# Kernel tuning notes

Measured on AMD Instinct MI355X. Metric: run time of the kernel, lower is better.

The kernel has to match this reference:

```python
import jax, jax.numpy as jnp
import numpy as np

N, F, DEG, C = 20000, 64, 16, 16   # nodes, features, in-degree incl. self loop, classes
E = N * (DEG - 1)                   # regular (non-self-loop) edges


def setup_inputs() -> dict:
    key = jax.random.key(0)
    ks = jax.random.split(key, 12)
    x = jax.random.normal(ks[0], (N, F), dtype=jnp.float32)
    src = jax.random.randint(ks[1], (E,), 0, N, dtype=jnp.int32)
    dst = jnp.repeat(jnp.arange(N, dtype=jnp.int32), DEG - 1)  # exactly DEG-1 in-edges/node
    edge_index = jnp.stack([src, dst])
    s = 1.0 / np.sqrt(F)
    params = {}
    for i, kw, kb in ((1, ks[2], ks[3]), (2, ks[4], ks[5]), (3, ks[6], ks[7])):
        params[f"W{i}"] = jax.random.normal(kw, (F, F), dtype=jnp.float32) * s
        params[f"b{i}"] = jax.random.normal(kb, (F,), dtype=jnp.float32) * s
    params["Wfc"] = jax.random.normal(ks[8], (C, F), dtype=jnp.float32) * s
    params["bfc"] = jax.random.normal(ks[9], (C,), dtype=jnp.float32) * s
    return {"x": x, "edge_index": edge_index, **params}


def _pca_conv(h, src, dst, W, b):
    # GCNConv.forward: linear first, then propagate with symmetric normalization.
    hl = h @ W.T                                             # [N, F]
    # add self loops (appended after regular edges, as in PyG)
    loop = jnp.arange(N, dtype=src.dtype)
    src_a = jnp.concatenate([src, loop])
    dst_a = jnp.concatenate([dst, loop])
    deg = jnp.zeros((N,), hl.dtype).at[dst_a].add(1.0)
    dinv = jax.lax.rsqrt(deg)
    norm = dinv[src_a] * dinv[dst_a]                         # [Ea]
    m = norm[:, None] * hl[src_a]                            # messages [Ea, F]
    # aggregate(): pack each destination's messages contiguously, in edge order
    order = jnp.argsort(dst_a)                               # stable sort by destination
    sd = dst_a[order]
    slot = jnp.arange(sd.shape[0]) - jnp.searchsorted(sd, sd, side='left')
    neigh = jnp.zeros((N, DEG, F), hl.dtype).at[sd, slot].set(m[order])
    neigh = neigh.reshape(N, DEG * F)                        # [N, max_degree*F]
    # torch.pca_lowrank(neigh, q=F, center=True): top-F right singular vectors of
    # the column-centered matrix; computed via eigh on the (DEG*F x DEG*F) Gram.
    Xc = neigh - jnp.mean(neigh, axis=0, keepdims=True)
    G = Xc.T @ Xc                                            # [DEG*F, DEG*F]
    _, V = jnp.linalg.eigh(G)                                # ascending eigenvalues
    Vtop = V[:, ::-1][:, :F]                                 # top-F principal directions
    proj = neigh @ Vtop                                      # note: projects UNcentered neigh
    return proj @ W.T + b                                    # self.lin again + bias


def reference(x, edge_index, W1, b1, W2, b2, W3, b3, Wfc, bfc):
    src, dst = edge_index[0], edge_index[1]
    h = jax.nn.relu(_pca_conv(x, src, dst, W1, b1))
    h = jax.nn.relu(_pca_conv(h, src, dst, W2, b2))
    h = jax.nn.relu(_pca_conv(h, src, dst, W3, b3))
    out = h @ Wfc.T + bfc
    return jax.nn.log_softmax(out, axis=-1)
```

## Files before the change

kernel.cpp:

```cpp
#include <hip/hip_runtime.h>
#include <cmath>

#define NNODES 20000
#define FD 64
#define EPN 15
#define NB 1024
#define BSUB 80
#define NCLS 16
#define NPAIR 40

__global__ __launch_bounds__(256) void k_linT(const float* __restrict__ X,
    const float* __restrict__ W, const float* __restrict__ bias,
    float* __restrict__ out, int ncol, int relu)
{
  __shared__ float Wsh[64][65];
  __shared__ float Xsh[64][65];
  int t = threadIdx.x;
  int r0 = blockIdx.x * 64;
  for (int idx = t; idx < ncol * 64; idx += 256) Wsh[idx >> 6][idx & 63] = W[idx];
  for (int idx = t; idx < 64 * 64; idx += 256) {
    int r = idx >> 6, c = idx & 63;
    Xsh[r][c] = (r0 + r < NNODES) ? X[(size_t)(r0 + r) * 64 + c] : 0.f;
  }
  __syncthreads();
  for (int idx = t; idx < 64 * ncol; idx += 256) {
    int r = idx / ncol, o = idx % ncol;
    float acc = 0.f;
    #pragma unroll
    for (int j = 0; j < 64; j++) acc += Xsh[r][j] * Wsh[o][j];
    if (bias) acc += bias[o];
    if (relu) acc = fmaxf(acc, 0.f);
    if (r0 + r < NNODES) out[(size_t)(r0 + r) * ncol + o] = acc;
  }
}

__global__ __launch_bounds__(256) void k_meanslot(const float* __restrict__ hl,
    const int* __restrict__ src, float* __restrict__ mus)
{
  int k = blockIdx.x;
  int part = blockIdx.y;
  int t = threadIdx.x;
  int c = t & 63, sub = t >> 6;
  int d0 = part * 2500;
  float acc = 0.f;
  for (int d = d0 + sub; d < d0 + 2500; d += 4) {
    int row = (k < EPN) ? src[d * EPN + k] : d;
    acc += hl[(size_t)row * 64 + c];
  }
  __shared__ float red[4][64];
  red[sub][c] = acc;
  __syncthreads();
  if (t < 64) {
    float s = red[0][t] + red[1][t] + red[2][t] + red[3][t];
    atomicAdd(&mus[k * 64 + t], s * (1.f / 20000.f));
  }
}

__global__ __launch_bounds__(256) void k_buildX(const float* __restrict__ hl,
    const int* __restrict__ src, const float* __restrict__ mus,
    float* __restrict__ X)
{
  __shared__ float4 mu4[256];
  int t = threadIdx.x;
  int d0 = blockIdx.x * 64;
  mu4[t] = ((const float4*)mus)[t];
  __syncthreads();
  for (int k = 0; k < 16; k++) {
    for (int item = t; item < 1024; item += 256) {
      int rr = item >> 4, f4 = item & 15;
      int d = d0 + rr;
      if (d < NNODES) {
        int row = (k < EPN) ? src[d * EPN + k] : d;
        float4 v = ((const float4*)hl)[(size_t)row * 16 + f4];
        float4 m = mu4[k * 16 + f4];
        v.x -= m.x; v.y -= m.y; v.z -= m.z; v.w -= m.w;
        ((float4*)X)[(size_t)d * 256 + k * 16 + f4] = v;
      }
    }
  }
}

__global__ __launch_bounds__(256) void k_syrkX(const float* __restrict__ X,
    float* __restrict__ TP, int rows)
{
  __shared__ float As[32][128];
  __shared__ float Bs[32][128];
  int t = threadIdx.x;
  int pr = blockIdx.x, I = 0, rem = pr;
  for (int ii = 0; ii < 8; ii++) {
    int cnt = 8 - ii;
    if (rem < cnt) { I = ii; break; }
    rem -= cnt;
  }
  int J = I + rem;
  int d0 = blockIdx.y * rows;
  int d1 = d0 + rows;
  int a0 = (t & 15) * 4, b0 = (t >> 4) * 4;
  float4 pa[4], pb[4];
  auto LOADR = [&](int dc) {
    #pragma unroll
    for (int s = 0; s < 4; s++) {
      int idx = t + s * 256;
      int rr = idx >> 5, c4 = idx & 31;
      int d = dc + rr;
      float4 va = make_float4(0.f, 0.f, 0.f, 0.f), vb = va;
      if (d < d1) {
        va = ((const float4*)X)[(size_t)d * 256 + I * 32 + c4];
        vb = ((const float4*)X)[(size_t)d * 256 + J * 32 + c4];
      }
      pa[s] = va; pb[s] = vb;
    }
  };
  LOADR(d0);
  float acc[8][8] = {};
  for (int dc = d0; dc < d1; dc += 32) {
    __syncthreads();
    #pragma unroll
    for (int s = 0; s < 4; s++) {
      int idx = t + s * 256;
      int rr = idx >> 5, c4 = idx & 31;
      *(float4*)&As[rr][c4 * 4] = pa[s];
      *(float4*)&Bs[rr][c4 * 4] = pb[s];
    }
    __syncthreads();
    if (dc + 32 < d1) LOADR(dc + 32);
    for (int dd = 0; dd < 32; dd++) {
      float av[8], bv[8];
      *(float4*)&av[0] = *(const float4*)&As[dd][a0];
      *(float4*)&av[4] = *(const float4*)&As[dd][a0 + 64];
      *(float4*)&bv[0] = *(const float4*)&Bs[dd][b0];
      *(float4*)&bv[4] = *(const float4*)&Bs[dd][b0 + 64];
      #pragma unroll
      for (int x = 0; x < 8; x++)
        #pragma unroll
        for (int y = 0; y < 8; y++) acc[x][y] += av[x] * bv[y];
    }
  }
  float* Tout = TP + (size_t)blockIdx.y * ((size_t)NB * NB);
  #pragma unroll
  for (int x = 0; x < 8; x++) {
    int rowi = I * 128 + ((x < 4) ? (a0 + x) : (64 + a0 + x - 4));
    size_t base = (size_t)rowi * NB + J * 128;
    *(float4*)&Tout[base + b0]      = make_float4(acc[x][0], acc[x][1], acc[x][2], acc[x][3]);
    *(float4*)&Tout[base + 64 + b0] = make_float4(acc[x][4], acc[x][5], acc[x][6], acc[x][7]);
  }
}

__global__ __launch_bounds__(256) void k_assembleG16(const float* __restrict__ TP,
    float* __restrict__ G, int ns)
{
  size_t idx = (size_t)blockIdx.x * 256 + threadIdx.x;
  int p = (int)(idx >> 10), q = (int)(idx & 1023);
  int ti = p >> 6, tj = q >> 6;
  size_t e = (ti <= tj) ? idx : (((size_t)q << 10) | (size_t)p);
  float v = 0.f;
  for (int s2 = 0; s2 < ns; s2++) v += TP[(size_t)s2 * ((size_t)NB * NB) + e];
  G[idx] = v * (1.f / 256.f);
}

__global__ __launch_bounds__(256) void k_gram(const float* __restrict__ hl,
    const int* __restrict__ src, const float* __restrict__ mus,
    float* __restrict__ T)
{
  __shared__ float Ash[64][64];
  __shared__ float Bsh[64][64];
  __shared__ float muA[64], muB[64];
  int t = threadIdx.x;
  int pr = blockIdx.x, i = 0, rem = pr;
  for (int ii = 0; ii < 16; ii++) {
    int cnt = 16 - ii;
    if (rem < cnt) { i = ii; break; }
    rem -= cnt;
  }
  int j = i + rem;
  if (t < 64) muA[t] = mus[i * 64 + t];
  else if (t < 128) muB[t - 64] = mus[j * 64 + (t - 64)];
  float acc[4][4] = {};
  int a0 = (t & 15) * 4, b0 = (t >> 4) * 4;
  int d0 = blockIdx.y * 4000, d1 = d0 + 4000;
  for (int dc = d0; dc < d1; dc += 64) {
    __syncthreads();
    for (int item = t; item < 1024; item += 256) {
      int rr = item >> 4, f4 = item & 15;
      int d = dc + rr;
      float4 va = make_float4(0.f, 0.f, 0.f, 0.f);
      float4 vb = va;
      if (d < d1) {
        int ra = (i < EPN) ? src[d * EPN + i] : d;
        int rb = (j < EPN) ? src[d * EPN + j] : d;
        va = ((const float4*)hl)[(size_t)ra * 16 + f4];
        vb = ((const float4*)hl)[(size_t)rb * 16 + f4];
        int cb = f4 * 4;
        va.x -= muA[cb]; va.y -= muA[cb + 1]; va.z -= muA[cb + 2]; va.w -= muA[cb + 3];
        vb.x -= muB[cb]; vb.y -= muB[cb + 1]; vb.z -= muB[cb + 2]; vb.w -= muB[cb + 3];
      }
      ((float4*)&Ash[rr][0])[f4] = va;
      ((float4*)&Bsh[rr][0])[f4] = vb;
    }
    __syncthreads();
    for (int dd = 0; dd < 64; dd++) {
      float av[4], bv[4];
      #pragma unroll
      for (int u = 0; u < 4; u++) av[u] = Ash[dd][a0 + u];
      #pragma unroll
      for (int u = 0; u < 4; u++) bv[u] = Bsh[dd][b0 + u];
      #pragma unroll
      for (int x = 0; x < 4; x++)
        #pragma unroll
        for (int y = 0; y < 4; y++) acc[x][y] += av[x] * bv[y];
    }
  }
  #pragma unroll
  for (int x = 0; x < 4; x++)
    #pragma unroll
    for (int y = 0; y < 4; y++)
      atomicAdd(&T[(size_t)(i * 64 + a0 + x) * NB + (j * 64 + b0 + y)], acc[x][y]);
}

__global__ __launch_bounds__(256) void k_assembleG(const float* __restrict__ T,
    float* __restrict__ G)
{
  size_t idx = (size_t)blockIdx.x * 256 + threadIdx.x;
  int p = (int)(idx >> 10), q = (int)(idx & 1023);
  int ti = p >> 6, tj = q >> 6;
  float v = (ti <= tj) ? T[idx] : T[((size_t)q << 10) | (size_t)p];
  G[idx] = v * (1.f / 256.f);
}

__global__ __launch_bounds__(256) void k_gemmG2(const float* __restrict__ G,
    float* __restrict__ G2)
{
  __shared__ float Ash[64][68];
  __shared__ float Bsh[64][68];
  int t = threadIdx.x;
  int bi = blockIdx.x * 64, bj = blockIdx.y * 64;
  int a0 = (t & 15) * 4, b0 = (t >> 4) * 4;
  float acc[4][4] = {};
  for (int d0 = 0; d0 < NB; d0 += 64) {
    __syncthreads();
    for (int item = t; item < 1024; item += 256) {
      int rr = item >> 4, f4 = item & 15;
      *(float4*)&Ash[rr][f4 * 4] =
          ((const float4*)G)[(size_t)(d0 + rr) * 256 + (bi >> 2) + f4];
      *(float4*)&Bsh[rr][f4 * 4] =
          ((const float4*)G)[(size_t)(d0 + rr) * 256 + (bj >> 2) + f4];
    }
    __syncthreads();
    for (int dd = 0; dd < 64; dd++) {
      float av[4], bv[4];
      #pragma unroll
      for (int u = 0; u < 4; u++) av[u] = Ash[dd][a0 + u];
      #pragma unroll
      for (int u = 0; u < 4; u++) bv[u] = Bsh[dd][b0 + u];
      #pragma unroll
      for (int x = 0; x < 4; x++)
        #pragma unroll
        for (int y = 0; y < 4; y++) acc[x][y] += av[x] * bv[y];
    }
  }
  #pragma unroll
  for (int x = 0; x < 4; x++) {
    float4 v = make_float4(acc[x][0], acc[x][1], acc[x][2], acc[x][3]);
    ((float4*)G2)[(size_t)(bi + a0 + x) * 256 + ((bj + b0) >> 2)] = v;
  }
}

__global__ void k_initScut(float* __restrict__ S, const float* __restrict__ G,
                           double* __restrict__ scal)
{
  int b = blockIdx.x;
  int t = threadIdx.x;
  if (b == 0) {
    __shared__ float red[256];
    float m = 0.f;
    for (int p = t; p < NB; p += 256) m = fmaxf(m, G[(size_t)p * NB + p]);
    red[t] = m;
    __syncthreads();
    for (int s = 128; s; s >>= 1) {
      if (t < s) red[t] = fmaxf(red[t], red[t + s]);
      __syncthreads();
    }
    if (t == 0) {
      double c = 0.9 * (double)red[0];
      scal[0] = c;
      scal[1] = c * c;
    }
    return;
  }
  int idx = (b - 1) * 256 + t;
  if (idx < NB * BSUB) {
    unsigned u = (unsigned)(idx + 1) * 2654435761u;
    u ^= u >> 16; u *= 2246822519u; u ^= u >> 13; u *= 3266489917u; u ^= u >> 16;
    S[idx] = ((float)u * (1.f / 4294967296.f)) - 0.5f;
  }
}

__global__ __launch_bounds__(256) void k_gzfused(const float* __restrict__ G,
    const float* __restrict__ Z, const float* __restrict__ Zp,
    float* __restrict__ P, float* __restrict__ out, int* __restrict__ cnt,
    const double* __restrict__ cptr, float s1, float s2, float s3)
{
  __shared__ float Gs[32][68];
  __shared__ float Zs[64][84];
  __shared__ int lastf;
  int t = threadIdx.x;
  int r0b = blockIdx.x;
  int r0 = r0b * 32;
  int kz = blockIdx.y;
  int cg = t & 15, rg = t >> 4;
  float acc0[5] = {}, acc1[5] = {};
  for (int k0 = kz * 128; k0 < kz * 128 + 128; k0 += 64) {
    __syncthreads();
    #pragma unroll
    for (int s = 0; s < 2; s++) {
      int item = t + s * 256;
      int rr = item >> 4, f4 = item & 15;
      float4 g = ((const float4*)G)[(size_t)(r0 + rr) * 256 + (k0 >> 2) + f4];
      *(float4*)&Gs[rr][f4 * 4] = g;
    }
    #pragma unroll
    for (int s = 0; s < 5; s++) {
      int item = t + s * 256;
      int rr = item / 20, f4 = item % 20;
      float4 z = ((const float4*)Z)[(size_t)(k0 + rr) * 20 + f4];
      *(float4*)&Zs[rr][f4 * 4] = z;
    }
    __syncthreads();
    for (int kk = 0; kk < 64; kk++) {
      float g0 = Gs[rg * 2 + 0][kk];
      float g1 = Gs[rg * 2 + 1][kk];
      float z[5];
      #pragma unroll
      for (int m = 0; m < 5; m++) z[m] = Zs[kk][cg * 5 + m];
      #pragma unroll
      for (int m = 0; m < 5; m++) { acc0[m] += g0 * z[m]; acc1[m] += g1 * z[m]; }
    }
  }
  size_t base = (size_t)kz * (NB * BSUB) + (size_t)(r0 + rg * 2) * BSUB + cg * 5;
  #pragma unroll
  for (int m = 0; m < 5; m++) P[base + m] = acc0[m];
  #pragma unroll
  for (int m = 0; m < 5; m++) P[base + BSUB + m] = acc1[m];
  __threadfence();
  __syncthreads();
  if (t == 0) {
    int old = atomicAdd(&cnt[r0b], 1);
    lastf = (old == 7) ? 1 : 0;
  }
  __syncthreads();
  if (!lastf) return;
  __threadfence();
  float coef = s1;
  if (cptr) coef = s1 * (float)(2.0 / cptr[0]);
  const float4* P4 = (const float4*)P;
  for (int idx = t; idx < 640; idx += 256) {
    size_t o4 = (size_t)r0 * 20 + idx;
    float4 a = P4[o4];
    #pragma unroll
    for (int u = 1; u < 8; u++) {
      float4 b = P4[(size_t)u * 20480 + o4];
      a.x += b.x; a.y += b.y; a.z += b.z; a.w += b.w;
    }
    float4 z = ((const float4*)Z)[o4];
    float4 o;
    o.x = coef * a.x + s2 * z.x;
    o.y = coef * a.y + s2 * z.y;
    o.z = coef * a.z + s2 * z.z;
    o.w = coef * a.w + s2 * z.w;
    if (s3 != 0.f) {
      float4 zp = ((const float4*)Zp)[o4];
      o.x += s3 * zp.x; o.y += s3 * zp.y; o.z += s3 * zp.z; o.w += s3 * zp.w;
    }
    ((float4*)out)[o4] = o;
  }
  __syncthreads();
  if (t == 0) cnt[r0b] = 0;
}

__global__ __launch_bounds__(512) void k_xtychol(const float* __restrict__ Sa,
    const float* __restrict__ Sb, double* __restrict__ CP,
    float* __restrict__ Rinv, int* __restrict__ cnt)
{
  __shared__ float Xsh[64][BSUB + 1];
  __shared__ float Ysh[64][BSUB + 1];
  __shared__ int lastf;
  int t = threadIdx.x;
  int i0 = blockIdx.x * 64;
  for (int idx = t; idx < 64 * BSUB; idx += 512) {
    int r = idx / BSUB, c = idx % BSUB;
    Xsh[r][c] = Sa[(size_t)(i0 + r) * BSUB + c];
    Ysh[r][c] = Sb[(size_t)(i0 + r) * BSUB + c];
  }
  __syncthreads();
  if (t < 256) {
    int a0 = (t & 15) * 5, b0 = (t >> 4) * 5;
    double acc[5][5] = {};
    for (int dd = 0; dd < 64; dd++) {
      float av[5], bv[5];
      #pragma unroll
      for (int u = 0; u < 5; u++) av[u] = Xsh[dd][a0 + u];
      #pragma unroll
      for (int u = 0; u < 5; u++) bv[u] = Ysh[dd][b0 + u];
      #pragma unroll
      for (int x = 0; x < 5; x++)
        #pragma unroll
        for (int y = 0; y < 5; y++) acc[x][y] += (double)av[x] * (double)bv[y];
    }
    double* outp = CP + (size_t)blockIdx.x * (BSUB * BSUB);
    #pragma unroll
    for (int x = 0; x < 5; x++)
      #pragma unroll
      for (int y = 0; y < 5; y++)
        outp[(size_t)(a0 + x) * BSUB + (b0 + y)] = acc[x][y];
  }
  __threadfence();
  __syncthreads();
  if (t == 0) lastf = (atomicAdd(&cnt[0], 1) == 15) ? 1 : 0;
  __syncthreads();
  if (!lastf) return;
  if (t == 0) cnt[0] = 0;
  __threadfence();
  __shared__ double R[BSUB][BSUB + 1];
  __shared__ double rownew[2][BSUB];
  __shared__ double dinv[BSUB];
  __shared__ float Xi[BSUB][BSUB + 1];
  for (int idx = t; idx < BSUB * BSUB; idx += 512) {
    double s = 0.0;
    #pragma unroll
    for (int b = 0; b < 16; b++) s += CP[(size_t)b * (BSUB * BSUB) + idx];
    R[idx / BSUB][idx % BSUB] = s;
  }
  __syncthreads();
  double flr0 = 1e-30 * (fabs(R[0][0]) + 1e-280);
  int prevrow = -1;
  int pb = 0;
  int k = 0;
  while (k < BSUB - 1) {
    int nrem = BSUB - 1 - k;
    int total = (nrem * (nrem + 1)) >> 1;
    int cplen = (prevrow >= 0) ? (BSUB - prevrow) : 0;
    double piv = R[k][k];
    if (piv < flr0) piv = flr0;
    double rp = 1.0 / piv;
    bool pair = (k + 1 < BSUB - 1);
    if (pair) {
      double dk1 = R[k][k + 1];
      double p1 = R[k + 1][k + 1] - dk1 * dk1 * rp;
      if (p1 < flr0) p1 = flr0;
      double rp1 = 1.0 / p1;
      for (int idx = t; idx < total + cplen; idx += 512) {
        if (idx < total) {
          float nf = 2.f * (float)nrem + 1.f;
          int a = (int)((nf - sqrtf(nf * nf - 8.f * (float)idx)) * 0.5f);
          while (a > 0 && a * nrem - ((a * (a - 1)) >> 1) > idx) a--;
          while ((a + 1) * nrem - (((a + 1) * a) >> 1) <= idx) a++;
          int off = idx - (a * nrem - ((a * (a - 1)) >> 1));
          int i2 = k + 1 + a, j2 = i2 + off;
          if (a == 0) {
            rownew[pb][j2] = R[k + 1][j2] - dk1 * R[k][j2] * rp;
          } else {
            double v = R[i2][j2] - R[k][i2] * R[k][j2] * rp;
            double R1i = R[k + 1][i2] - dk1 * R[k][i2] * rp;
            double R1j = R[k + 1][j2] - dk1 * R[k][j2] * rp;
            v -= R1i * R1j * rp1;
            R[i2][j2] = v;
          }
        } else {
          int j = prevrow + (idx - total);
          R[prevrow][j] = rownew[pb ^ 1][j];
        }
      }
      __syncthreads();
      prevrow = k + 1; pb ^= 1; k += 2;
    } else {
      for (int idx = t; idx < total + cplen; idx += 512) {
        if (idx < total) {
          float nf = 2.f * (float)nrem + 1.f;
          int a = (int)((nf - sqrtf(nf * nf - 8.f * (float)idx)) * 0.5f);
          while (a > 0 && a * nrem - ((a * (a - 1)) >> 1) > idx) a--;
          while ((a + 1) * nrem - (((a + 1) * a) >> 1) <= idx) a++;
          int off = idx - (a * nrem - ((a * (a - 1)) >> 1));
          int i2 = k + 1 + a, j2 = i2 + off;
          R[i2][j2] -= R[k][i2] * R[k][j2] * rp;
        } else {
          int j = prevrow + (idx - total);
          R[prevrow][j] = rownew[pb ^ 1][j];
        }
      }
      __syncthreads();
      prevrow = -1; k += 1;
    }
  }
  if (prevrow >= 0) {
    for (int j = prevrow + t; j < BSUB; j += 512) R[prevrow][j] = rownew[pb ^ 1][j];
    __syncthreads();
  }
  if (t < BSUB) {
    double piv = R[t][t];
    if (piv < flr0) piv = flr0;
    dinv[t] = 1.0 / sqrt(piv);
  }
  __syncthreads();
  for (int idx = t; idx < BSUB * BSUB; idx += 512) {
    int kk = idx / BSUB, j = idx % BSUB;
    if (j > kk) R[kk][j] *= dinv[kk];
  }
  __syncthreads();
  if (t < BSUB) R[t][t] = 1.0 / dinv[t];
  __syncthreads();
  if (t < BSUB) {
    int j = t;
    Xi[j][j] = (float)dinv[j];
    for (int i = j - 1; i >= 0; i--) {
      double s = 0.0;
      for (int k2 = i + 1; k2 <= j; k2++) s += R[i][k2] * (double)Xi[k2][j];
      Xi[i][j] = (float)(-s * dinv[i]);
    }
    for (int i = j + 1; i < BSUB; i++) Xi[i][j] = 0.f;
  }
  __syncthreads();
  for (int idx = t; idx < BSUB * BSUB; idx += 512)
    Rinv[idx] = Xi[idx / BSUB][idx % BSUB];
}

__global__ __launch_bounds__(256) void k_gemmSR(const float* __restrict__ S,
    const float* __restrict__ Rinv, float* __restrict__ out)
{
  __shared__ float Rsh[BSUB][84];
  int t = threadIdx.x;
  for (int idx = t; idx < BSUB * BSUB; idx += 256)
    Rsh[idx / BSUB][idx % BSUB] = Rinv[idx];
  __syncthreads();
  int r0 = blockIdx.x * 32;
  int r = t >> 3, c0 = (t & 7) * 10;
  float acc[10] = {};
  const float* srow = &S[(size_t)(r0 + r) * BSUB];
  for (int k = 0; k < BSUB; k++) {
    float s = srow[k];
    #pragma unroll
    for (int m = 0; m < 10; m++) acc[m] += s * Rsh[k][c0 + m];
  }
  #pragma unroll
  for (int m = 0; m < 10; m++) out[(size_t)(r0 + r) * BSUB + c0 + m] = acc[m];
}

__global__ __launch_bounds__(1024) void k_xtyjac(const float* __restrict__ Sa,
    const float* __restrict__ Sb, double* __restrict__ CP,
    float* __restrict__ Uout, int* __restrict__ perm,
    double* __restrict__ cutout, int sweeps, int withU, int* __restrict__ cnt)
{
  __shared__ float Xsh[64][BSUB + 1];
  __shared__ float Ysh[64][BSUB + 1];
  __shared__ int lastf;
  int t = threadIdx.x;
  int i0 = blockIdx.x * 64;
  for (int idx = t; idx < 64 * BSUB; idx += 1024) {
    int r = idx / BSUB, c = idx % BSUB;
    Xsh[r][c] = Sa[(size_t)(i0 + r) * BSUB + c];
    Ysh[r][c] = Sb[(size_t)(i0 + r) * BSUB + c];
  }
  __syncthreads();
  if (t < 256) {
    int a0 = (t & 15) * 5, b0 = (t >> 4) * 5;
    double acc[5][5] = {};
    for (int dd = 0; dd < 64; dd++) {
      float av[5], bv[5];
      #pragma unroll
      for (int u = 0; u < 5; u++) av[u] = Xsh[dd][a0 + u];
      #pragma unroll
      for (int u = 0; u < 5; u++) bv[u] = Ysh[dd][b0 + u];
      #pragma unroll
      for (int x = 0; x < 5; x++)
        #pragma unroll
        for (int y = 0; y < 5; y++) acc[x][y] += (double)av[x] * (double)bv[y];
    }
    double* outp = CP + (size_t)blockIdx.x * (BSUB * BSUB);
    #pragma unroll
    for (int x = 0; x < 5; x++)
      #pragma unroll
      for (int y = 0; y < 5; y++)
        outp[(size_t)(a0 + x) * BSUB + (b0 + y)] = acc[x][y];
  }
  __threadfence();
  __syncthreads();
  if (t == 0) lastf = (atomicAdd(&cnt[0], 1) == 15) ? 1 : 0;
  __syncthreads();
  if (!lastf) return;
  if (t == 0) cnt[0] = 0;
  __threadfence();
  __shared__ float Mb[2][BSUB][BSUB + 1];
  __shared__ float Ut[BSUB][BSUB];
  __shared__ float4 rot[2][NPAIR];
  __shared__ float th[BSUB];
  __shared__ int id[BSUB];
  for (int idx = t; idx < BSUB * BSUB; idx += 1024) {
    double s = 0.0;
    #pragma unroll
    for (int b = 0; b < 16; b++) s += CP[(size_t)b * (BSUB * BSUB) + idx];
    Mb[1][idx / BSUB][idx % BSUB] = (float)s;
    if (withU) Ut[idx / BSUB][idx % BSUB] = ((idx / BSUB) == (idx % BSUB)) ? 1.f : 0.f;
  }
  int pr0 = t / 40, j0 = t - pr0 * 40;
  int pr1 = -1, j1 = 0;
  {
    int i1 = t + 1024;
    if (i1 < 1600) { pr1 = i1 / 40; j1 = i1 - pr1 * 40; }
  }
  int upr0 = -1, um0 = 0, upr1 = -1, um1 = 0;
  if (t >= 40) {
    int u0 = t - 40;              upr0 = u0 / 40; um0 = u0 - upr0 * 40;
    int u1 = t - 40 + 984;
    if (u1 < 1600) { upr1 = u1 / 40; um1 = u1 - upr1 * 40; }
  }
  int rp_ = 0, rq_ = 0;
  if (t < 40) {
    rp_ = (t == 0) ? 0 : 1 + (t - 1) % 79;
    rq_ = 1 + (78 - t) % 79;
  }
  __syncthreads();
  for (int idx = t; idx < BSUB * BSUB; idx += 1024) {
    int i2 = idx / BSUB, j2 = idx % BSUB;
    Mb[0][i2][j2] = 0.5f * (Mb[1][i2][j2] + Mb[1][j2][i2]);
  }
  __syncthreads();
  int nrounds = sweeps * (BSUB - 1);
  int mcur = 0;
  for (int it = 0; it < nrounds; it++) {
    int pb = it & 1;
    float (*Mc)[BSUB + 1] = Mb[mcur];
    float (*Mn)[BSUB + 1] = Mb[mcur ^ 1];
    if (t < 40) {
      int p = rp_, q = rq_;
      if (p > q) { int tmp = p; p = q; q = tmp; }
      float apq = Mc[p][q];
      float c = 1.f, s = 0.f;
      if (fabsf(apq) > 1e-28f) {
        float tau = (Mc[q][q] - Mc[p][p]) / (2.f * apq);
        float tt = copysignf(1.f, tau) / (fabsf(tau) + sqrtf(1.f + tau * tau));
        c = rsqrtf(1.f + tt * tt);
        s = tt * c;
      }
      rot[pb][t] = make_float4(c, s, __int_as_float(p), __int_as_float(q));
      if (t > 0) rp_ = (rp_ == 79) ? 1 : rp_ + 1;
      rq_ = (rq_ == 79) ? 1 : rq_ + 1;
    } else if (withU && it > 0) {
      int ob = pb ^ 1;
      {
        float4 R0 = rot[ob][upr0];
        int p = __float_as_int(R0.z), q = __float_as_int(R0.w);
        float c = R0.x, s = R0.y;
        float2 up = *(float2*)&Ut[p][2 * um0];
        float2 uq = *(float2*)&Ut[q][2 * um0];
        float2 np, nq;
        np.x = c * up.x - s * uq.x;  np.y = c * up.y - s * uq.y;
        nq.x = s * up.x + c * uq.x;  nq.y = s * up.y + c * uq.y;
        *(float2*)&Ut[p][2 * um0] = np;
        *(float2*)&Ut[q][2 * um0] = nq;
      }
      if (upr1 >= 0) {
        float4 R1 = rot[ob][upr1];
        int p = __float_as_int(R1.z), q = __float_as_int(R1.w);
        float c = R1.x, s = R1.y;
        float2 up = *(float2*)&Ut[p][2 * um1];
        float2 uq = *(float2*)&Ut[q][2 * um1];
        float2 np, nq;
        np.x = c * up.x - s * uq.x;  np.y = c * up.y - s * uq.y;
        nq.x = s * up.x + c * uq.x;  nq.y = s * up.y + c * uq.y;
        *(float2*)&Ut[p][2 * um1] = np;
        *(float2*)&Ut[q][2 * um1] = nq;
      }
    }
    __syncthreads();
    {
      float4 Rp = rot[pb][pr0];
      float4 Rj = rot[pb][j0];
      int p = __float_as_int(Rp.z), q = __float_as_int(Rp.w);
      float c = Rp.x, s = Rp.y;
      int k = __float_as_int(Rj.z), k2 = __float_as_int(Rj.w);
      float cj = Rj.x, sj = Rj.y;
      float mpk = Mc[p][k],  mqk = Mc[q][k];
      float mpk2 = Mc[p][k2], mqk2 = Mc[q][k2];
      float rpk  = c * mpk  - s * mqk;
      float rqk  = s * mpk  + c * mqk;
      float rpk2 = c * mpk2 - s * mqk2;
      float rqk2 = s * mpk2 + c * mqk2;
      Mn[p][k]  = cj * rpk - sj * rpk2;
      Mn[q][k]  = cj * rqk - sj * rqk2;
      Mn[p][k2] = sj * rpk + cj * rpk2;
      Mn[q][k2] = sj * rqk + cj * rqk2;
    }
    if (pr1 >= 0) {
      float4 Rp = rot[pb][pr1];
      float4 Rj = rot[pb][j1];
      int p = __float_as_int(Rp.z), q = __float_as_int(Rp.w);
      float c = Rp.x, s = Rp.y;
      int k = __float_as_int(Rj.z), k2 = __float_as_int(Rj.w);
      float cj = Rj.x, sj = Rj.y;
      float mpk = Mc[p][k],  mqk = Mc[q][k];
      float mpk2 = Mc[p][k2], mqk2 = Mc[q][k2];
      float rpk  = c * mpk  - s * mqk;
      float rqk  = s * mpk  + c * mqk;
      float rpk2 = c * mpk2 - s * mqk2;
      float rqk2 = s * mpk2 + c * mqk2;
      Mn[p][k]  = cj * rpk - sj * rpk2;
      Mn[q][k]  = cj * rqk - sj * rqk2;
      Mn[p][k2] = sj * rpk + cj * rpk2;
      Mn[q][k2] = sj * rqk + cj * rqk2;
    }
    __syncthreads();
    mcur ^= 1;
  }
  if (withU) {
    int ob = (nrounds - 1) & 1;
    {
      float4 R0 = rot[ob][pr0];
      int p = __float_as_int(R0.z), q = __float_as_int(R0.w);
      float c = R0.x, s = R0.y;
      float2 up = *(float2*)&Ut[p][2 * j0];
      float2 uq = *(float2*)&Ut[q][2 * j0];
      float2 np, nq;
      np.x = c * up.x - s * uq.x;  np.y = c * up.y - s * uq.y;
      nq.x = s * up.x + c * uq.x;  nq.y = s * up.y + c * uq.y;
      *(float2*)&Ut[p][2 * j0] = np;
      *(float2*)&Ut[q][2 * j0] = nq;
    }
    if (pr1 >= 0) {
      float4 R1 = rot[ob][pr1];
      int p = __float_as_int(R1.z), q = __float_as_int(R1.w);
      float c = R1.x, s = R1.y;
      float2 up = *(float2*)&Ut[p][2 * j1];
      float2 uq = *(float2*)&Ut[q][2 * j1];
      float2 np, nq;
      np.x = c * up.x - s * uq.x;  np.y = c * up.y - s * uq.y;
      nq.x = s * up.x + c * uq.x;  nq.y = s * up.y + c * uq.y;
      *(float2*)&Ut[p][2 * j1] = np;
      *(float2*)&Ut[q][2 * j1] = nq;
    }
    __syncthreads();
  }
  float (*Mf)[BSUB + 1] = Mb[mcur];
  if (t < BSUB) { th[t] = Mf[t][t]; id[t] = t; }
  __syncthreads();
  if (t == 0) {
    for (int a = 1; a < BSUB; a++) {
      float v = th[a]; int ii = id[a]; int b = a - 1;
      while (b >= 0 && th[b] < v) { th[b + 1] = th[b]; id[b + 1] = id[b]; b--; }
      th[b + 1] = v; id[b + 1] = ii;
    }
    double cut = (double)th[BSUB - 1];
    double lo = 0.02 * (double)th[0];
    if (cut < lo) cut = lo;
    double hi = 0.98 * (double)th[63];
    if (cut > hi) cut = hi;
    cutout[0] = cut;
    cutout[1] = cut * cut;
  }
  __syncthreads();
  if (t < BSUB) perm[t] = id[t];
  if (withU)
    for (int idx = t; idx < BSUB * BSUB; idx += 1024) {
      int k = idx / BSUB, p = idx % BSUB;
      Uout[idx] = Ut[p][k];
    }
}

__global__ __launch_bounds__(256) void k_compose(const float* __restrict__ S,
    const float* __restrict__ U, const int* __restrict__ perm,
    float* __restrict__ out)
{
  __shared__ float Ush[BSUB][65];
  int t = threadIdx.x;
  for (int idx = t; idx < BSUB * 64; idx += 256) {
    int jj = idx >> 6, c = idx & 63;
    Ush[jj][c] = U[jj * BSUB + perm[c]];
  }
  __syncthreads();
  int r0 = blockIdx.x * 64;
  for (int oidx = t; oidx < 64 * 64; oidx += 256) {
    int r = oidx >> 6, c = oidx & 63;
    float acc = 0.f;
    const float* srow = &S[(size_t)(r0 + r) * BSUB];
    #pragma unroll 8
    for (int j = 0; j < BSUB; j++) acc += srow[j] * Ush[j][c];
    out[(size_t)(r0 + r) * 64 + c] = acc;
  }
}

__global__ __launch_bounds__(256) void k_projlin(const float* __restrict__ hl,
    const int* __restrict__ src, const float* __restrict__ Vtop,
    const float* __restrict__ W, const float* __restrict__ bias,
    float* __restrict__ hout)
{
  __shared__ float Vsh[64][68];
  __shared__ float Hsh[64][68];
  __shared__ float Psh[64][68];
  int t = threadIdx.x;
  int d0 = blockIdx.x * 64;
  int dd = t & 63, pg = t >> 6;
  float acc[16] = {};
  for (int k = 0; k < 16; k++) {
    __syncthreads();
    for (int item = t; item < 1024; item += 256) {
      int rr = item >> 4, f4 = item & 15;
      *(float4*)&Vsh[rr][f4 * 4] = ((const float4*)Vtop)[(size_t)(k * 64 + rr) * 16 + f4];
      int d = d0 + rr;
      float4 v = make_float4(0.f, 0.f, 0.f, 0.f);
      if (d < NNODES) {
        int row = (k < EPN) ? src[d * EPN + k] : d;
        v = ((const float4*)hl)[(size_t)row * 16 + f4];
      }
      *(float4*)&Hsh[rr][f4 * 4] = v;
    }
    __syncthreads();
    for (int j = 0; j < 64; j++) {
      float h = Hsh[dd][j];
      #pragma unroll
      for (int m = 0; m < 16; m++) acc[m] += h * Vsh[j][pg * 16 + m];
    }
  }
  __syncthreads();
  #pragma unroll
  for (int m = 0; m < 16; m++) Psh[dd][pg * 16 + m] = acc[m] * (1.f / 16.f);
  for (int item = t; item < 1024; item += 256) {
    int rr = item >> 4, f4 = item & 15;
    *(float4*)&Vsh[rr][f4 * 4] = ((const float4*)W)[(size_t)rr * 16 + f4];
  }
  __syncthreads();
  if (d0 + dd < NNODES) {
    #pragma unroll
    for (int m = 0; m < 16; m++) {
      int o = pg * 16 + m;
      float a = bias[o];
      for (int j = 0; j < 64; j++) a += Psh[dd][j] * Vsh[o][j];
      hout[(size_t)(d0 + dd) * 64 + o] = fmaxf(a, 0.f);
    }
  }
}

__global__ void k_logsoftmax(const float* __restrict__ logits, float* __restrict__ out)
{
  int n = blockIdx.x * 256 + threadIdx.x;
  if (n >= NNODES) return;
  float v[NCLS];
  float mx = -1e30f;
  #pragma unroll
  for (int c = 0; c < NCLS; c++) { v[c] = logits[(size_t)n * NCLS + c]; mx = fmaxf(mx, v[c]); }
  float se = 0.f;
  #pragma unroll
  for (int c = 0; c < NCLS; c++) se += expf(v[c] - mx);
  float lse = mx + logf(se);
  #pragma unroll
  for (int c = 0; c < NCLS; c++) out[(size_t)n * NCLS + c] = v[c] - lse;
}

extern "C" void kernel_launch(void* const* d_in, const int* in_sizes, int n_in,
                              void* d_out, int out_size, void* d_ws, size_t ws_size,
                              hipStream_t stream)
{
  (void)in_sizes; (void)n_in; (void)out_size;
  const float* x = (const float*)d_in[0];
  const int* src = (const int*)d_in[1];
  const float* Wl[3] = { (const float*)d_in[2], (const float*)d_in[4], (const float*)d_in[6] };
  const float* bl[3] = { (const float*)d_in[3], (const float*)d_in[5], (const float*)d_in[7] };
  const float* Wfc = (const float*)d_in[8];
  const float* bfc = (const float*)d_in[9];
  float* outp = (float*)d_out;

  char* w = (char*)d_ws;
  auto alloc = [&](size_t bytes) -> char* {
    char* p = w; w += (bytes + 255) & ~(size_t)255; return p;
  };
  float* hA   = (float*)alloc((size_t)NNODES * 64 * 4);
  float* hB   = (float*)alloc((size_t)NNODES * 64 * 4);
  float* hl   = (float*)alloc((size_t)NNODES * 64 * 4);
  float* T    = (float*)alloc((size_t)NB * NB * 4);
  float* G    = (float*)alloc((size_t)NB * NB * 4);
  float* G2   = (float*)alloc((size_t)NB * NB * 4);
  float* mus  = (float*)alloc(16 * 64 * 4);
  float* Zb[6];
  for (int i = 0; i < 6; i++) Zb[i] = (float*)alloc((size_t)NB * BSUB * 4);
  float* P     = (float*)alloc((size_t)8 * NB * BSUB * 4);
  int* cnt     = (int*)alloc(64 * 4);
  double* CP   = (double*)alloc((size_t)16 * BSUB * BSUB * 8);
  float* Rinv  = (float*)alloc(BSUB * BSUB * 4);
  float* U     = (float*)alloc(BSUB * BSUB * 4);
  int* perm    = (int*)alloc(BSUB * 4);
  float* Vtop  = (float*)alloc((size_t)NB * 64 * 4);
  double* scal = (double*)alloc(16 * 8);
  float* X      = (float*)alloc((size_t)NNODES * NB * 4);
  float* TP     = (float*)alloc((size_t)16 * (size_t)NB * NB * 4);
  size_t used16 = (size_t)(w - (char*)d_ws);
  (void)alloc((size_t)4 * (size_t)NB * NB * 4);
  size_t used20 = (size_t)(w - (char*)d_ws);
  int fastg = (used16 <= ws_size) ? 1 : 0;
  int NS    = (used20 <= ws_size) ? 20 : 16;

  const int GRID_ROWS = (NNODES + 63) / 64;

  hipMemsetAsync(cnt, 0, 64 * 4, stream);

  int cur = 0;
  auto gemmGZ = [&](const float* A, const float* Z, const float* Zp, float* o,
                    const double* cptr, float s1, float s2, float s3) {
    hipLaunchKernelGGL(k_gzfused, dim3(32, 8), dim3(256), 0, stream,
                       A, Z, Zp, P, o, cnt, cptr, s1, s2, s3);
  };
  auto chunk2 = [&](int deg, const double* cptr) {
    int a = (cur + 1) % 6, b = (cur + 2) % 6;
    float* bufs[3] = { Zb[cur], Zb[a], Zb[b] };
    int ip = 0, ic = 0, io = 1;
    for (int s = 0; s < deg; s++) {
      if (s == 0)
        gemmGZ(G2, bufs[ic], nullptr, bufs[io], cptr, 1.f, -1.f, 0.f);
      else
        gemmGZ(G2, bufs[ic], bufs[ip], bufs[io], cptr, 2.f, -2.f, -1.f);
      if (s == 0) { ip = 0; ic = 1; io = 2; }
      else { int tmp = ip; ip = ic; ic = io; io = tmp; }
    }
    int sel = (deg - 1) % 3;
    cur = (sel == 0) ? a : (sel == 1) ? b : cur;
  };
  auto cholqr = [&]() {
    hipLaunchKernelGGL(k_xtychol, dim3(16), dim3(512), 0, stream,
                       Zb[cur], Zb[cur], CP, Rinv, cnt + 32);
    int o = (cur + 1) % 6;
    hipLaunchKernelGGL(k_gemmSR, dim3(32), dim3(256), 0, stream, Zb[cur], Rinv, Zb[o]);
    cur = o;
  };
  auto rrmid = [&](double* cutp) {
    int y = (cur + 1) % 6;
    gemmGZ(G, Zb[cur], nullptr, Zb[y], nullptr, 1.f, 0.f, 0.f);
    hipLaunchKernelGGL(k_xtyjac, dim3(16), dim3(1024), 0, stream,
                       Zb[cur], Zb[y], CP, U, perm, cutp, 2, 0, cnt + 33);
  };
  auto rrfinal = [&](double* cutp) {
    int y = (cur + 1) % 6;
    gemmGZ(G, Zb[cur], nullptr, Zb[y], nullptr, 1.f, 0.f, 0.f);
    hipLaunchKernelGGL(k_xtyjac, dim3(16), dim3(1024), 0, stream,
                       Zb[cur], Zb[y], CP, U, perm, cutp, 5, 1, cnt + 33);
    hipLaunchKernelGGL(k_compose, dim3(16), dim3(256), 0, stream,
                       Zb[cur], U, perm, Vtop);
  };

  const float* hin = x;
  float* hout = hA;
  for (int l = 0; l < 3; l++) {
    hipLaunchKernelGGL(k_linT, dim3(GRID_ROWS), dim3(256), 0, stream,
                       hin, Wl[l], (const float*)nullptr, hl, 64, 0);
    hipMemsetAsync(mus, 0, 16 * 64 * 4, stream);
    hipLaunchKernelGGL(k_meanslot, dim3(16, 8), dim3(256), 0, stream, hl, src, mus);
    if (fastg) {
      hipLaunchKernelGGL(k_buildX, dim3(GRID_ROWS), dim3(256), 0, stream,
                         hl, src, mus, X);
      hipLaunchKernelGGL(k_syrkX, dim3(36, NS), dim3(256), 0, stream,
                         X, TP, NNODES / NS);
      hipLaunchKernelGGL(k_assembleG16, dim3(4096), dim3(256), 0, stream, TP, G, NS);
    } else {
      hipMemsetAsync(T, 0, (size_t)NB * NB * 4, stream);
      hipLaunchKernelGGL(k_gram, dim3(136, 5), dim3(256), 0, stream, hl, src, mus, T);
      hipLaunchKernelGGL(k_assembleG, dim3(4096), dim3(256), 0, stream, T, G);
    }
    hipLaunchKernelGGL(k_gemmG2, dim3(16, 16), dim3(256), 0, stream, G, G2);
    cur = 0;
    hipLaunchKernelGGL(k_initScut, dim3(1 + (NB * BSUB + 255) / 256), dim3(256), 0,
                       stream, Zb[cur], G, scal);
    chunk2(6, &scal[1]); cholqr();
    rrmid(&scal[2]);
    chunk2(7, &scal[3]); cholqr();
    chunk2(7, &scal[3]); cholqr();
    rrfinal(&scal[4]);
    hipLaunchKernelGGL(k_projlin, dim3(GRID_ROWS), dim3(256), 0, stream,
                       hl, src, Vtop, Wl[l], bl[l], hout);
    hin = hout;
    hout = (hout == hA) ? hB : hA;
  }
  hipLaunchKernelGGL(k_linT, dim3(GRID_ROWS), dim3(256), 0, stream,
                     hin, Wfc, bfc, hl, NCLS, 0);
  hipLaunchKernelGGL(k_logsoftmax, dim3((NNODES + 255) / 256), dim3(256), 0, stream,
                     hl, outp);
}
```

Measured before the change: 8.855 ms.

## Run Chebyshev filter chain as one persistent cooperative kernel with grid syncs

Replaces the per-step k_gzfused launches in chunk2 with a single cooperative kernel of 256 blocks. It loops over all polynomial degrees and uses grid.sync between the partial GEMM and the reduce/combine stage. This removes launch overhead and the atomic-counter last-block reduction, and spreads the reduction work across all blocks. In exchange it adds two grid-wide barriers per step and relaxed atomic loads and stores for Z and P. It falls back to the old path if the cooperative launch fails.

```diff
diff --git a/kernel.cpp b/kernel.cpp
--- a/kernel.cpp
+++ b/kernel.cpp
@@ -1,5 +1,8 @@
 #include <hip/hip_runtime.h>
+#include <hip/hip_cooperative_groups.h>
 #include <cmath>
+
+namespace cg = cooperative_groups;
 
 #define NNODES 20000
 #define FD 64
@@ -8,6 +11,13 @@
 #define BSUB 80
 #define NCLS 16
 #define NPAIR 40
+
+__device__ __forceinline__ float cload(const float* p) {
+  return __hip_atomic_load(p, __ATOMIC_RELAXED, __HIP_MEMORY_SCOPE_AGENT);
+}
+__device__ __forceinline__ void cstore(float* p, float v) {
+  __hip_atomic_store(p, v, __ATOMIC_RELAXED, __HIP_MEMORY_SCOPE_AGENT);
+}
 
 __global__ __launch_bounds__(256) void k_linT(const float* __restrict__ X,
     const float* __restrict__ W, const float* __restrict__ bias,
@@ -307,7 +317,7 @@
   int r0b = blockIdx.x;
   int r0 = r0b * 32;
   int kz = blockIdx.y;
-  int cg = t & 15, rg = t >> 4;
+  int cg_ = t & 15, rg = t >> 4;
   float acc0[5] = {}, acc1[5] = {};
   for (int k0 = kz * 128; k0 < kz * 128 + 128; k0 += 64) {
     __syncthreads();
@@ -331,12 +341,12 @@
       float g1 = Gs[rg * 2 + 1][kk];
       float z[5];
       #pragma unroll
-      for (int m = 0; m < 5; m++) z[m] = Zs[kk][cg * 5 + m];
+      for (int m = 0; m < 5; m++) z[m] = Zs[kk][cg_ * 5 + m];
       #pragma unroll
       for (int m = 0; m < 5; m++) { acc0[m] += g0 * z[m]; acc1[m] += g1 * z[m]; }
     }
   }
-  size_t base = (size_t)kz * (NB * BSUB) + (size_t)(r0 + rg * 2) * BSUB + cg * 5;
+  size_t base = (size_t)kz * (NB * BSUB) + (size_t)(r0 + rg * 2) * BSUB + cg_ * 5;
   #pragma unroll
   for (int m = 0; m < 5; m++) P[base + m] = acc0[m];
   #pragma unroll
@@ -375,6 +385,84 @@
   }
   __syncthreads();
   if (t == 0) cnt[r0b] = 0;
+}
+
+__global__ __launch_bounds__(256) void k_gzchain(const float* __restrict__ G,
+    float* b0_, float* b1_, float* b2_, float* __restrict__ P,
+    const double* __restrict__ cptr, int deg)
+{
+  __shared__ float Gs[32][68];
+  __shared__ float Zs[64][84];
+  cg::grid_group grid = cg::this_grid();
+  int t = threadIdx.x;
+  int blk = blockIdx.x;
+  int r0b = blk >> 3;
+  int kz  = blk & 7;
+  int r0 = r0b * 32;
+  int cg_ = t & 15, rg = t >> 4;
+  float* bufs[3] = { b0_, b1_, b2_ };
+  float base = (float)(2.0 / cptr[0]);
+  int ip = 0, ic = 0, io = 1;
+  for (int s = 0; s < deg; s++) {
+    const float* Z = bufs[ic];
+    float acc0[5] = {}, acc1[5] = {};
+    for (int k0 = kz * 128; k0 < kz * 128 + 128; k0 += 64) {
+      __syncthreads();
+      #pragma unroll
+      for (int u = 0; u < 2; u++) {
+        int item = t + u * 256;
+        int rr = item >> 4, f4 = item & 15;
+        float4 g = ((const float4*)G)[(size_t)(r0 + rr) * 256 + (k0 >> 2) + f4];
+        *(float4*)&Gs[rr][f4 * 4] = g;
+      }
+      #pragma unroll
+      for (int u = 0; u < 5; u++) {
+        int item = t + u * 256;
+        int rr = item / 20, c4 = item % 20;
+        const float* zp = &Z[(size_t)(k0 + rr) * 20 * 4 + c4 * 4];
+        float4 z = make_float4(cload(zp), cload(zp + 1), cload(zp + 2), cload(zp + 3));
+        *(float4*)&Zs[rr][c4 * 4] = z;
+      }
+      __syncthreads();
+      for (int kk = 0; kk < 64; kk++) {
+        float g0 = Gs[rg * 2 + 0][kk];
+        float g1 = Gs[rg * 2 + 1][kk];
+        float z[5];
+        #pragma unroll
+        for (int m = 0; m < 5; m++) z[m] = Zs[kk][cg_ * 5 + m];
+        #pragma unroll
+        for (int m = 0; m < 5; m++) { acc0[m] += g0 * z[m]; acc1[m] += g1 * z[m]; }
+      }
+    }
+    size_t pbase = (size_t)kz * (NB * BSUB) + (size_t)(r0 + rg * 2) * BSUB + cg_ * 5;
+    #pragma unroll
+    for (int m = 0; m < 5; m++) cstore(&P[pbase + m], acc0[m]);
+    #pragma unroll
+    for (int m = 0; m < 5; m++) cstore(&P[pbase + BSUB + m], acc1[m]);
+    __threadfence();
+    grid.sync();
+    float s1 = (s == 0) ? 1.f : 2.f;
+    float s2 = (s == 0) ? -1.f : -2.f;
+    float s3 = (s == 0) ? 0.f : -1.f;
+    float coef = s1 * base;
+    const float* Zp = bufs[ip];
+    float* Out = bufs[io];
+    for (int idx = t; idx < 320; idx += 256) {
+      int row = r0 + kz * 4 + idx / 80;
+      int col = idx % 80;
+      size_t o = (size_t)row * BSUB + col;
+      float a = 0.f;
+      #pragma unroll
+      for (int u = 0; u < 8; u++) a += cload(&P[(size_t)u * (NB * BSUB) + o]);
+      float v = coef * a + s2 * cload(&Z[o]);
+      if (s > 0) v += s3 * cload(&Zp[o]);
+      cstore(&Out[o], v);
+    }
+    __threadfence();
+    grid.sync();
+    if (s == 0) { ip = 0; ic = 1; io = 2; }
+    else { int tmp = ip; ip = ic; ic = io; io = tmp; }
+  }
 }
 
 __global__ __launch_bounds__(512) void k_xtychol(const float* __restrict__ Sa,
@@ -900,6 +988,7 @@
   hipMemsetAsync(cnt, 0, 64 * 4, stream);
 
   int cur = 0;
+  int coopOK = 1;
   auto gemmGZ = [&](const float* A, const float* Z, const float* Zp, float* o,
                     const double* cptr, float s1, float s2, float s3) {
     hipLaunchKernelGGL(k_gzfused, dim3(32, 8), dim3(256), 0, stream,
@@ -908,14 +997,30 @@
   auto chunk2 = [&](int deg, const double* cptr) {
     int a = (cur + 1) % 6, b = (cur + 2) % 6;
     float* bufs[3] = { Zb[cur], Zb[a], Zb[b] };
-    int ip = 0, ic = 0, io = 1;
-    for (int s = 0; s < deg; s++) {
-      if (s == 0)
-        gemmGZ(G2, bufs[ic], nullptr, bufs[io], cptr, 1.f, -1.f, 0.f);
-      else
-        gemmGZ(G2, bufs[ic], bufs[ip], bufs[io], cptr, 2.f, -2.f, -1.f);
-      if (s == 0) { ip = 0; ic = 1; io = 2; }
-      else { int tmp = ip; ip = ic; ic = io; io = tmp; }
+    int launched = 0;
+    if (coopOK) {
+      const float* gg = G2;
+      float* b0 = bufs[0]; float* b1 = bufs[1]; float* b2 = bufs[2];
+      float* pp = P;
+      const double* cp = cptr;
+      int dd = deg;
+      void* args[] = { (void*)&gg, (void*)&b0, (void*)&b1, (void*)&b2,
+                       (void*)&pp, (void*)&cp, (void*)&dd };
+      hipError_t e = hipLaunchCooperativeKernel(
+          reinterpret_cast<void*>(k_gzchain), dim3(256), dim3(256), args, 0, stream);
+      if (e == hipSuccess) launched = 1;
+      else coopOK = 0;
+    }
+    if (!launched) {
+      int ip = 0, ic = 0, io = 1;
+      for (int s = 0; s < deg; s++) {
+        if (s == 0)
+          gemmGZ(G2, bufs[ic], nullptr, bufs[io], cptr, 1.f, -1.f, 0.f);
+        else
+          gemmGZ(G2, bufs[ic], bufs[ip], bufs[io], cptr, 2.f, -2.f, -1.f);
+        if (s == 0) { ip = 0; ic = 1; io = 2; }
+        else { int tmp = ip; ip = ic; ic = io; io = tmp; }
+      }
     }
     int sel = (deg - 1) % 3;
     cur = (sel == 0) ? a : (sel == 1) ? b : cur;
```

Measured after the change: 13.33 ms. 1.51x slower.
